# Optimization experiments

Measured on AMD Instinct MI355X. Metric: run time of the kernel, lower is better.

Reference implementation:

```python
import jax, jax.numpy as jnp
import numpy as np

NUM_HEADS = 8

def _qkv(t, W, b, H):
    # t: [B, L, C] -> q, k, v each [B, H, L, D]
    B, L, C = t.shape
    D = C // H
    qkv = (t @ W + b).reshape(B, L, 3, H, D)
    qkv = jnp.moveaxis(qkv, 2, 0)           # [3, B, L, H, D]
    qkv = jnp.swapaxes(qkv, 2, 3)           # [3, B, H, L, D]
    return qkv[0], qkv[1], qkv[2]

def _attend(q, k, v, scale):
    # q,k,v: [B, H, L, D] -> [B, L, C]
    B, H, L, D = q.shape
    scores = jnp.einsum('bhqd,bhkd->bhqk', q, k) * scale
    attn = jax.nn.softmax(scores, axis=-1)
    out = jnp.einsum('bhqk,bhkd->bhqd', attn, v)
    return jnp.swapaxes(out, 1, 2).reshape(B, L, H * D)

def setup_inputs() -> dict:
    key = jax.random.key(0)
    ks = jax.random.split(key, 7)
    B, N, C = 8, 2048, 512
    s_in = 1.0 / np.sqrt(C)
    return {
        'x': jax.random.normal(ks[0], (B, N, C), dtype=jnp.float32),
        'W_rgb_qkv': jax.random.normal(ks[1], (C, 3 * C), dtype=jnp.float32) * s_in,
        'b_rgb_qkv': jax.random.normal(ks[2], (3 * C,), dtype=jnp.float32) * 0.02,
        'W_depth_qkv': jax.random.normal(ks[3], (C, 3 * C), dtype=jnp.float32) * s_in,
        'b_depth_qkv': jax.random.normal(ks[4], (3 * C,), dtype=jnp.float32) * 0.02,
        'W_proj': jax.random.normal(ks[5], (C, C), dtype=jnp.float32) * s_in,
        'b_proj': jax.random.normal(ks[6], (C,), dtype=jnp.float32) * 0.02,
    }

def reference(x, W_rgb_qkv, b_rgb_qkv, W_depth_qkv, b_depth_qkv, W_proj, b_proj):
    B, N, C = x.shape
    H = NUM_HEADS
    D = C // H
    scale = D ** -0.5
    L = N // 2
    rgb, depth = x[:, :L], x[:, L:]
    rq, rk, rv = _qkv(rgb, W_rgb_qkv, b_rgb_qkv, H)
    dq, dk, dv = _qkv(depth, W_depth_qkv, b_depth_qkv, H)
    # rgb queries attend to depth K/V (named depth_v in torch code)
    depth_out = _attend(rq, dk, dv, scale)
    # depth queries attend to rgb K/V (named rgb_v in torch code)
    rgb_out = _attend(dq, rk, rv, scale)
    out = jnp.concatenate([rgb_out, depth_out], axis=1)  # [B, N, C]
    return out @ W_proj + b_proj
```

## Files before the change

kernel.cpp:

```cpp
#include <hip/hip_runtime.h>
#include <hip/hip_bf16.h>

typedef __attribute__((ext_vector_type(8))) short s16x8;
typedef __attribute__((ext_vector_type(4))) float f32x4;

__device__ __forceinline__ ushort f2bf(float f) {
  union { float f; unsigned int u; } c; c.f = f;
  unsigned int u = c.u + 0x7fffu + ((c.u >> 16) & 1u);
  return (ushort)(u >> 16);
}

__device__ __forceinline__ unsigned int pack2(float lo, float hi) {
  __hip_bfloat162 b2 = __float22bfloat162_rn(make_float2(lo, hi));
  union { __hip_bfloat162 b; unsigned int u; } c; c.b = b2;
  return c.u;
}

__device__ __forceinline__ s16x8 ld16(const ushort* p) {
  union { uint4 u; s16x8 s; } c;
  c.u = *reinterpret_cast<const uint4*>(p);
  return c.s;
}

__device__ __forceinline__ f32x4 mfma16(s16x8 a, s16x8 b, f32x4 c) {
  return __builtin_amdgcn_mfma_f32_16x16x32_bf16(a, b, c, 0, 0, 0);
}

__device__ __forceinline__ float exp2fast(float x) { return __builtin_amdgcn_exp2f(x); }

__device__ __forceinline__ void gld_lds16(const void* g, void* l) {
  __builtin_amdgcn_global_load_lds(
      (const __attribute__((address_space(1))) void*)g,
      (__attribute__((address_space(3))) void*)l, 16, 0, 0);
}


__global__ __launch_bounds__(256) void k_prep(
    const float* __restrict__ x, ushort* __restrict__ xb,
    const float* __restrict__ Wr, ushort* __restrict__ WtR,
    const float* __restrict__ Wd, ushort* __restrict__ WtD,
    const float* __restrict__ Wp, ushort* __restrict__ WtP) {
  __shared__ float tile[32][33];
  int b = blockIdx.x, t = threadIdx.x;
  if (b < 8192) {
    int i = (b * 256 + t) * 4;
    float4 v = *reinterpret_cast<const float4*>(x + i);
    ushort4 o;
    o.x = f2bf(v.x); o.y = f2bf(v.y); o.z = f2bf(v.z); o.w = f2bf(v.w);
    *reinterpret_cast<ushort4*>(xb + i) = o;
    return;
  }
  b -= 8192;
  const float* src; ushort* dst; int N;
  if (b < 768)      { src = Wr; dst = WtR; N = 1536; }
  else if (b < 1536){ b -= 768;  src = Wd; dst = WtD; N = 1536; }
  else              { b -= 1536; src = Wp; dst = WtP; N = 512; }
  int nb = N >> 5;
  int n0 = (b % nb) * 32, k0 = (b / nb) * 32;
  int tx = t & 31, ty = t >> 5;
#pragma unroll
  for (int i = 0; i < 32; i += 8)
    tile[ty + i][tx] = src[(k0 + ty + i) * N + (n0 + tx)];
  __syncthreads();
#pragma unroll
  for (int i = 0; i < 32; i += 8)
    dst[(size_t)(n0 + ty + i) * 512 + (k0 + tx)] = f2bf(tile[tx][ty + i]);
}


__device__ __forceinline__ void stage_lds(const ushort* __restrict__ src, int ld,
                                          char* ldsbase, int t) {
#pragma unroll
  for (int p = 0; p < 4; ++p) {
    int chunk = p * 256 + t;
    int r = chunk >> 3, cc = chunk & 7;
    gld_lds16(src + r * ld + ((cc ^ (r & 7)) * 8), ldsbase + (chunk & ~63) * 16);
  }
}

__device__ __forceinline__ s16x8 lds_frag(const char* lds, int row, int c) {
  union { uint4 u; s16x8 s; } cv;
  cv.u = *reinterpret_cast<const uint4*>(lds + row * 128 + ((c ^ (row & 7)) * 16));
  return cv.s;
}


__global__ __launch_bounds__(256) void k_qkv(
    const ushort* __restrict__ xb, const ushort* __restrict__ WtR,
    const ushort* __restrict__ WtD, const float* __restrict__ bR,
    const float* __restrict__ bD, ushort* __restrict__ Qb,
    ushort* __restrict__ Kb, ushort* __restrict__ Vt) {
  __shared__ __align__(16) char lds[32768];
  char* ldsA = lds;
  char* ldsB = lds + 16384;
  int m0 = blockIdx.x * 128;
  int n0 = blockIdx.y * 128;
  bool TRANS = n0 >= 1024;
  int s = m0 >> 13, bb = (m0 >> 10) & 7, lbase = m0 & 1023;
  const ushort* A = xb + (size_t)(bb * 2048 + s * 1024 + lbase) * 512;
  const ushort* Wt = (s ? WtD : WtR) + (size_t)n0 * 512;
  const float* bias = s ? bD : bR;
  int t = threadIdx.x;
  int wid = t >> 6, ln = t & 15, g = (t & 63) >> 4;
  int wr = wid >> 1, wc = wid & 1;
  f32x4 acc[4][4] = {};
  for (int ks = 0; ks < 8; ++ks) {
    __syncthreads();
    stage_lds(A + ks * 64, 512, ldsA, t);
    stage_lds(Wt + ks * 64, 512, ldsB, t);
    __syncthreads();
#pragma unroll
    for (int kk = 0; kk < 2; ++kk) {
      s16x8 af[4], bf[4];
#pragma unroll
      for (int mi = 0; mi < 4; ++mi) af[mi] = lds_frag(ldsA, wr * 64 + mi * 16 + ln, kk * 4 + g);
#pragma unroll
      for (int ni = 0; ni < 4; ++ni) bf[ni] = lds_frag(ldsB, wc * 64 + ni * 16 + ln, kk * 4 + g);
      if (TRANS) {
#pragma unroll
        for (int mi = 0; mi < 4; ++mi)
#pragma unroll
          for (int ni = 0; ni < 4; ++ni) acc[mi][ni] = mfma16(bf[ni], af[mi], acc[mi][ni]);
      } else {
#pragma unroll
        for (int mi = 0; mi < 4; ++mi)
#pragma unroll
          for (int ni = 0; ni < 4; ++ni) acc[mi][ni] = mfma16(af[mi], bf[ni], acc[mi][ni]);
      }
    }
  }
  int hb_base = (s * 8 + bb) * 8;
  if (!TRANS) {
    bool isK = (n0 >> 9) != 0;
    ushort* dst = isK ? Kb : Qb;
    float sc = isK ? 1.0f : 0.18033688011112042f;
#pragma unroll
    for (int mi = 0; mi < 4; ++mi)
#pragma unroll
      for (int ni = 0; ni < 4; ++ni) {
        f32x4 v = acc[mi][ni];
        int col = n0 + wc * 64 + ni * 16 + ln;
        int h = (col >> 6) & 7, d = col & 63;
        float bv = bias[col];
        ushort* hp = dst + ((size_t)(hb_base + h) << 16);
        int lr = lbase + wr * 64 + mi * 16 + g * 4;
#pragma unroll
        for (int j = 0; j < 4; ++j) hp[(lr + j) * 64 + d] = f2bf((v[j] + bv) * sc);
      }
  } else {
#pragma unroll
    for (int mi = 0; mi < 4; ++mi)
#pragma unroll
      for (int ni = 0; ni < 4; ++ni) {
        f32x4 v = acc[mi][ni];
        int nb = n0 + wc * 64 + ni * 16 + g * 4;
        int mm = m0 + wr * 64 + mi * 16 + ln;
        int l = mm & 1023;
        int lp = (l & ~63) | (l & 0x23) | ((l & 0x0C) << 1) | ((l & 0x10) >> 2);
#pragma unroll
        for (int j = 0; j < 4; ++j) {
          int col = nb + j;
          int h = (col >> 6) & 7, d = col & 63;
          Vt[((size_t)(hb_base + h) << 16) + d * 1024 + lp] = f2bf(v[j] + bias[col]);
        }
      }
  }
}


__global__ __launch_bounds__(256, 4) void k_attn(const ushort* __restrict__ Qb,
                                                 const ushort* __restrict__ Kb,
                                                 const ushort* __restrict__ Vt,
                                                 ushort* __restrict__ AO) {
  __shared__ __align__(16) char lds[32768];
  int bid = blockIdx.x;
  int set = bid & 127, qb = bid >> 7;
  int pair = set & 1, h = (set >> 1) & 7, bb = set >> 4;
  int sQ = 1 - pair, sKV = pair;
  const ushort* Qp = Qb + ((size_t)((sQ * 8 + bb) * 8 + h) << 16);
  const ushort* Kp = Kb + ((size_t)((sKV * 8 + bb) * 8 + h) << 16);
  const ushort* Vp = Vt + ((size_t)((sKV * 8 + bb) * 8 + h) << 16);
  int t = threadIdx.x, w = t >> 6, l = t & 63, ln = t & 15, g = (t & 63) >> 4;
  int q0 = qb * 128 + w * 32;
  s16x8 qf0a = ld16(Qp + (q0 + ln) * 64 + g * 8);
  s16x8 qf1a = ld16(Qp + (q0 + ln) * 64 + 32 + g * 8);
  s16x8 qf0b = ld16(Qp + (q0 + 16 + ln) * 64 + g * 8);
  s16x8 qf1b = ld16(Qp + (q0 + 16 + ln) * 64 + 32 + g * 8);

  int cA = w * 128 + l;
  int cB = w * 128 + 64 + l;
  int rA = cA >> 3, ccA = cA & 7;
  int rB = cB >> 3, ccB = cB & 7;
  int kofA = rA * 64 + ((ccA ^ (rA & 7)) * 8);
  int kofB = rB * 64 + ((ccB ^ (rB & 7)) * 8);
  int vofA = rA * 1024 + ((ccA ^ (rA & 7)) * 8);
  int vofB = rB * 1024 + ((ccB ^ (rB & 7)) * 8);

  float ls_a = 0.f, ls_b = 0.f;
  f32x4 oca[4] = {}, ocb[4] = {};

  {
    char* base = lds;
    gld_lds16(Kp + kofA, base + w * 2048);
    gld_lds16(Kp + kofB, base + w * 2048 + 1024);
    gld_lds16(Vp + vofA, base + 8192 + w * 2048);
    gld_lds16(Vp + vofB, base + 8192 + w * 2048 + 1024);
  }
  __syncthreads();

  int cur = 0;
  for (int it = 0; it < 16; ++it) {
    int t0 = it * 64;
    if (it < 15) {
      char* base = lds + (cur ^ 1) * 16384;
      const ushort* kp = Kp + (t0 + 64) * 64;
      const ushort* vp = Vp + (t0 + 64);
      gld_lds16(kp + kofA, base + w * 2048);
      gld_lds16(kp + kofB, base + w * 2048 + 1024);
      gld_lds16(vp + vofA, base + 8192 + w * 2048);
      gld_lds16(vp + vofB, base + 8192 + w * 2048 + 1024);
    }
    const char* ldsK = lds + cur * 16384;
    const char* ldsV = ldsK + 8192;

    f32x4 za[4], zb[4];
#pragma unroll
    for (int s = 0; s < 4; ++s) {
      s16x8 k0 = lds_frag(ldsK, s * 16 + ln, g);
      s16x8 k1 = lds_frag(ldsK, s * 16 + ln, 4 + g);
      f32x4 z1 = {}; z1 = mfma16(k0, qf0a, z1); z1 = mfma16(k1, qf1a, z1); za[s] = z1;
      f32x4 z2 = {}; z2 = mfma16(k0, qf0b, z2); z2 = mfma16(k1, qf1b, z2); zb[s] = z2;
    }

    unsigned int pwa[8], pwb[8];
#pragma unroll
    for (int s = 0; s < 4; ++s) {
      float p0 = exp2fast(za[s][0]), p1 = exp2fast(za[s][1]);
      float p2 = exp2fast(za[s][2]), p3 = exp2fast(za[s][3]);
      ls_a += (p0 + p1) + (p2 + p3);
      pwa[2 * s] = pack2(p0, p1); pwa[2 * s + 1] = pack2(p2, p3);
      float r0 = exp2fast(zb[s][0]), r1 = exp2fast(zb[s][1]);
      float r2 = exp2fast(zb[s][2]), r3 = exp2fast(zb[s][3]);
      ls_b += (r0 + r1) + (r2 + r3);
      pwb[2 * s] = pack2(r0, r1); pwb[2 * s + 1] = pack2(r2, r3);
    }
    union { uint4 u; s16x8 v; } c0, c1, c2, c3;
    c0.u = make_uint4(pwa[0], pwa[1], pwa[2], pwa[3]);
    c1.u = make_uint4(pwa[4], pwa[5], pwa[6], pwa[7]);
    c2.u = make_uint4(pwb[0], pwb[1], pwb[2], pwb[3]);
    c3.u = make_uint4(pwb[4], pwb[5], pwb[6], pwb[7]);
    s16x8 pf0a = c0.v, pf1a = c1.v, pf0b = c2.v, pf1b = c3.v;

#pragma unroll
    for (int d = 0; d < 4; ++d) {
      s16x8 v0 = lds_frag(ldsV, d * 16 + ln, g);
      s16x8 v1 = lds_frag(ldsV, d * 16 + ln, 4 + g);
      oca[d] = mfma16(v0, pf0a, oca[d]);
      oca[d] = mfma16(v1, pf1a, oca[d]);
      ocb[d] = mfma16(v0, pf0b, ocb[d]);
      ocb[d] = mfma16(v1, pf1b, ocb[d]);
    }
    __syncthreads();
    cur ^= 1;
  }

  ls_a += __shfl_xor(ls_a, 16, 64);
  ls_a += __shfl_xor(ls_a, 32, 64);
  ls_b += __shfl_xor(ls_b, 16, 64);
  ls_b += __shfl_xor(ls_b, 32, 64);
  float inva = 1.0f / ls_a, invb = 1.0f / ls_b;
  int orow = bb * 2048 + pair * 1024 + q0 + ln;
#pragma unroll
  for (int d = 0; d < 4; ++d) {
    uint2 st;
    st.x = pack2(oca[d][0] * inva, oca[d][1] * inva);
    st.y = pack2(oca[d][2] * inva, oca[d][3] * inva);
    *reinterpret_cast<uint2*>(AO + (size_t)orow * 512 + h * 64 + d * 16 + 4 * g) = st;
    uint2 st2;
    st2.x = pack2(ocb[d][0] * invb, ocb[d][1] * invb);
    st2.y = pack2(ocb[d][2] * invb, ocb[d][3] * invb);
    *reinterpret_cast<uint2*>(AO + (size_t)(orow + 16) * 512 + h * 64 + d * 16 + 4 * g) = st2;
  }
}


__global__ __launch_bounds__(256) void k_gemm_proj(const ushort* __restrict__ AO,
                                                   const ushort* __restrict__ WtP,
                                                   const float* __restrict__ bP,
                                                   float* __restrict__ Out) {
  __shared__ __align__(16) char lds[32768];
  char* ldsA = lds;
  char* ldsB = lds + 16384;
  int m0 = blockIdx.x * 128, n0 = blockIdx.y * 128;
  const ushort* A = AO + (size_t)m0 * 512;
  const ushort* Wt = WtP + (size_t)n0 * 512;
  int t = threadIdx.x;
  int wid = t >> 6, ln = t & 15, g = (t & 63) >> 4;
  int wr = wid >> 1, wc = wid & 1;
  f32x4 acc[4][4] = {};
  for (int ks = 0; ks < 8; ++ks) {
    __syncthreads();
    stage_lds(A + ks * 64, 512, ldsA, t);
    stage_lds(Wt + ks * 64, 512, ldsB, t);
    __syncthreads();
#pragma unroll
    for (int kk = 0; kk < 2; ++kk) {
      s16x8 af[4], bf[4];
#pragma unroll
      for (int mi = 0; mi < 4; ++mi) af[mi] = lds_frag(ldsA, wr * 64 + mi * 16 + ln, kk * 4 + g);
#pragma unroll
      for (int ni = 0; ni < 4; ++ni) bf[ni] = lds_frag(ldsB, wc * 64 + ni * 16 + ln, kk * 4 + g);
#pragma unroll
      for (int mi = 0; mi < 4; ++mi)
#pragma unroll
        for (int ni = 0; ni < 4; ++ni) acc[mi][ni] = mfma16(af[mi], bf[ni], acc[mi][ni]);
    }
  }
#pragma unroll
  for (int mi = 0; mi < 4; ++mi)
#pragma unroll
    for (int ni = 0; ni < 4; ++ni) {
      f32x4 v = acc[mi][ni];
      int col = n0 + wc * 64 + ni * 16 + ln;
      float bv = bP[col];
      int r0 = m0 + wr * 64 + mi * 16 + g * 4;
#pragma unroll
      for (int j = 0; j < 4; ++j) Out[(size_t)(r0 + j) * 512 + col] = v[j] + bv;
    }
}


extern "C" void kernel_launch(void* const* d_in, const int* in_sizes, int n_in,
                              void* d_out, int out_size, void* d_ws, size_t ws_size,
                              hipStream_t stream) {
  const float* x      = (const float*)d_in[0];
  const float* W_rgb  = (const float*)d_in[1];
  const float* b_rgb  = (const float*)d_in[2];
  const float* W_dep  = (const float*)d_in[3];
  const float* b_dep  = (const float*)d_in[4];
  const float* W_proj = (const float*)d_in[5];
  const float* b_proj = (const float*)d_in[6];
  float* out = (float*)d_out;

  char* ws = (char*)d_ws;
  ushort* xb  = (ushort*)(ws + 0);
  ushort* WtR = (ushort*)(ws + 16777216);
  ushort* WtD = (ushort*)(ws + 18350080);
  ushort* WtP = (ushort*)(ws + 19922944);
  ushort* Qb  = (ushort*)(ws + 20447232);
  ushort* Kb  = (ushort*)(ws + 37224448);
  ushort* Vt  = (ushort*)(ws + 54001664);
  ushort* AO  = (ushort*)(ws + 70778880);

  k_prep<<<9984, 256, 0, stream>>>(x, xb, W_rgb, WtR, W_dep, WtD, W_proj, WtP);
  k_qkv<<<dim3(128, 12), 256, 0, stream>>>(xb, WtR, WtD, b_rgb, b_dep, Qb, Kb, Vt);
  k_attn<<<1024, 256, 0, stream>>>(Qb, Kb, Vt, AO);
  k_gemm_proj<<<dim3(128, 4), 256, 0, stream>>>(AO, WtP, b_proj, out);
}
```

Before: 142.3 us.

## Double-buffer LDS in GEMM kernels, split QKV launch by transpose mode

Both the QKV and projection GEMMs now stage the next K-slice into a second LDS buffer while the current one feeds the MFMAs, which replaces two barriers per iteration with one and overlaps global loads with compute. The QKV kernel becomes a template on the transpose flag and is launched twice, once for Q/K and once for V, so the runtime branch is gone. Doubling LDS to 64KB per block may cut occupancy. The attention kernel's launch bound rises to 5 blocks per CU, which tightens the register budget.

```diff
diff --git a/kernel.cpp b/kernel.cpp
--- a/kernel.cpp
+++ b/kernel.cpp
@@ -85,17 +85,15 @@
 }
 
 
+template <bool TRANS>
 __global__ __launch_bounds__(256) void k_qkv(
     const ushort* __restrict__ xb, const ushort* __restrict__ WtR,
     const ushort* __restrict__ WtD, const float* __restrict__ bR,
     const float* __restrict__ bD, ushort* __restrict__ Qb,
     ushort* __restrict__ Kb, ushort* __restrict__ Vt) {
-  __shared__ __align__(16) char lds[32768];
-  char* ldsA = lds;
-  char* ldsB = lds + 16384;
+  __shared__ __align__(16) char lds[65536];
   int m0 = blockIdx.x * 128;
-  int n0 = blockIdx.y * 128;
-  bool TRANS = n0 >= 1024;
+  int n0 = (TRANS ? 1024 : 0) + blockIdx.y * 128;
   int s = m0 >> 13, bb = (m0 >> 10) & 7, lbase = m0 & 1023;
   const ushort* A = xb + (size_t)(bb * 2048 + s * 1024 + lbase) * 512;
   const ushort* Wt = (s ? WtD : WtR) + (size_t)n0 * 512;
@@ -104,11 +102,18 @@
   int wid = t >> 6, ln = t & 15, g = (t & 63) >> 4;
   int wr = wid >> 1, wc = wid & 1;
   f32x4 acc[4][4] = {};
+  stage_lds(A, 512, lds, t);
+  stage_lds(Wt, 512, lds + 16384, t);
+  __syncthreads();
   for (int ks = 0; ks < 8; ++ks) {
-    __syncthreads();
-    stage_lds(A + ks * 64, 512, ldsA, t);
-    stage_lds(Wt + ks * 64, 512, ldsB, t);
-    __syncthreads();
+    char* cbuf = lds + (ks & 1) * 32768;
+    if (ks < 7) {
+      char* nbuf = lds + ((ks + 1) & 1) * 32768;
+      stage_lds(A + (ks + 1) * 64, 512, nbuf, t);
+      stage_lds(Wt + (ks + 1) * 64, 512, nbuf + 16384, t);
+    }
+    char* ldsA = cbuf;
+    char* ldsB = cbuf + 16384;
 #pragma unroll
     for (int kk = 0; kk < 2; ++kk) {
       s16x8 af[4], bf[4];
@@ -116,18 +121,14 @@
       for (int mi = 0; mi < 4; ++mi) af[mi] = lds_frag(ldsA, wr * 64 + mi * 16 + ln, kk * 4 + g);
 #pragma unroll
       for (int ni = 0; ni < 4; ++ni) bf[ni] = lds_frag(ldsB, wc * 64 + ni * 16 + ln, kk * 4 + g);
-      if (TRANS) {
-#pragma unroll
-        for (int mi = 0; mi < 4; ++mi)
-#pragma unroll
-          for (int ni = 0; ni < 4; ++ni) acc[mi][ni] = mfma16(bf[ni], af[mi], acc[mi][ni]);
-      } else {
-#pragma unroll
-        for (int mi = 0; mi < 4; ++mi)
-#pragma unroll
-          for (int ni = 0; ni < 4; ++ni) acc[mi][ni] = mfma16(af[mi], bf[ni], acc[mi][ni]);
-      }
-    }
+#pragma unroll
+      for (int mi = 0; mi < 4; ++mi)
+#pragma unroll
+        for (int ni = 0; ni < 4; ++ni)
+          acc[mi][ni] = TRANS ? mfma16(bf[ni], af[mi], acc[mi][ni])
+                              : mfma16(af[mi], bf[ni], acc[mi][ni]);
+    }
+    __syncthreads();
   }
   int hb_base = (s * 8 + bb) * 8;
   if (!TRANS) {
@@ -168,7 +169,7 @@
 }
 
 
-__global__ __launch_bounds__(256, 4) void k_attn(const ushort* __restrict__ Qb,
+__global__ __launch_bounds__(256, 5) void k_attn(const ushort* __restrict__ Qb,
                                                  const ushort* __restrict__ Kb,
                                                  const ushort* __restrict__ Vt,
                                                  ushort* __restrict__ AO) {
@@ -288,9 +289,7 @@
                                                    const ushort* __restrict__ WtP,
                                                    const float* __restrict__ bP,
                                                    float* __restrict__ Out) {
-  __shared__ __align__(16) char lds[32768];
-  char* ldsA = lds;
-  char* ldsB = lds + 16384;
+  __shared__ __align__(16) char lds[65536];
   int m0 = blockIdx.x * 128, n0 = blockIdx.y * 128;
   const ushort* A = AO + (size_t)m0 * 512;
   const ushort* Wt = WtP + (size_t)n0 * 512;
@@ -298,11 +297,18 @@
   int wid = t >> 6, ln = t & 15, g = (t & 63) >> 4;
   int wr = wid >> 1, wc = wid & 1;
   f32x4 acc[4][4] = {};
+  stage_lds(A, 512, lds, t);
+  stage_lds(Wt, 512, lds + 16384, t);
+  __syncthreads();
   for (int ks = 0; ks < 8; ++ks) {
-    __syncthreads();
-    stage_lds(A + ks * 64, 512, ldsA, t);
-    stage_lds(Wt + ks * 64, 512, ldsB, t);
-    __syncthreads();
+    char* cbuf = lds + (ks & 1) * 32768;
+    if (ks < 7) {
+      char* nbuf = lds + ((ks + 1) & 1) * 32768;
+      stage_lds(A + (ks + 1) * 64, 512, nbuf, t);
+      stage_lds(Wt + (ks + 1) * 64, 512, nbuf + 16384, t);
+    }
+    char* ldsA = cbuf;
+    char* ldsB = cbuf + 16384;
 #pragma unroll
     for (int kk = 0; kk < 2; ++kk) {
       s16x8 af[4], bf[4];
@@ -315,6 +321,7 @@
 #pragma unroll
         for (int ni = 0; ni < 4; ++ni) acc[mi][ni] = mfma16(af[mi], bf[ni], acc[mi][ni]);
     }
+    __syncthreads();
   }
 #pragma unroll
   for (int mi = 0; mi < 4; ++mi)
@@ -353,7 +360,8 @@
   ushort* AO  = (ushort*)(ws + 70778880);
 
   k_prep<<<9984, 256, 0, stream>>>(x, xb, W_rgb, WtR, W_dep, WtD, W_proj, WtP);
-  k_qkv<<<dim3(128, 12), 256, 0, stream>>>(xb, WtR, WtD, b_rgb, b_dep, Qb, Kb, Vt);
+  k_qkv<false><<<dim3(128, 8), 256, 0, stream>>>(xb, WtR, WtD, b_rgb, b_dep, Qb, Kb, Vt);
+  k_qkv<true><<<dim3(128, 4), 256, 0, stream>>>(xb, WtR, WtD, b_rgb, b_dep, Qb, Kb, Vt);
   k_attn<<<1024, 256, 0, stream>>>(Qb, Kb, Vt, AO);
   k_gemm_proj<<<dim3(128, 4), 256, 0, stream>>>(AO, WtP, b_proj, out);
 }
```

Result: slower. 161.1 us (+13.2%).
